# Optimization experiments

Hardware: AMD Instinct MI355X
Metric: run time of the kernel (lower is better)

Reference implementation:

```python
import jax, jax.numpy as jnp
import numpy as np

B, N_PIC, C, H, W, P = 32, 4, 3, 224, 224, 16
HP = H // P  # 14
NP = HP * HP  # 196 patches
D = C * P * P  # 768 = hidden_size


def setup_inputs() -> dict:
    key = jax.random.key(0)
    ks = jax.random.split(key, 12)
    s = 0.02
    def lin(k, din, dout):
        kw, kb = jax.random.split(k)
        return (jax.random.normal(kw, (din, dout), jnp.float32) * s,
                jax.random.normal(kb, (dout,), jnp.float32) * s)
    W1, b1 = lin(ks[0], D, D)
    Wq, bq = lin(ks[1], D, D)
    Wk, bk = lin(ks[2], D, D)
    Wv, bv = lin(ks[3], D, D)
    Wo1, bo1 = lin(ks[4], D, D)
    Wo2, bo2 = lin(ks[5], D, D)
    x = jax.random.normal(ks[6], (B, N_PIC, C, H, W), jnp.float32)
    return {"x": x, "W1": W1, "b1": b1, "Wq": Wq, "bq": bq, "Wk": Wk,
            "bk": bk, "Wv": Wv, "bv": bv, "Wo1": Wo1, "bo1": bo1,
            "Wo2": Wo2, "bo2": bo2}


def reference(x, W1, b1, Wq, bq, Wk, bk, Wv, bv, Wo1, bo1, Wo2, bo2):
    b = x.shape[0]
    # patchify: matches torch unfold(3,P,P).unfold(4,P,P) + permute + view
    # -> [b, N, num_patches, C*P*P] with (C, ph, pw) ordering in last dim
    p = x.reshape(b, N_PIC, C, HP, P, HP, P)
    p = p.transpose(0, 1, 3, 5, 2, 4, 6).reshape(b, N_PIC, NP, D)
    h = p @ W1 + b1  # [b, N, S, D]
    # attention: query always from picture 0; key/value per picture (batched)
    Q = h[:, 0] @ Wq + bq          # [b, S, D]
    K = h @ Wk + bk                # [b, N, S, D]
    V = h @ Wv + bv                # [b, N, S, D]
    scale = 1.0 / jnp.sqrt(jnp.float32(D))
    scores = jnp.einsum('bsd,bnmd->bnsm', Q, K) * scale  # [b, N, S, S]
    attn = jax.nn.softmax(scores, axis=-1)
    wv = jnp.einsum('bnsm,bnmd->bnsd', attn, V)           # [b, N, S, D]
    out = jax.nn.relu(wv @ Wo1 + bo1) @ Wo2 + bo2
    return out
```

## Files before the change

### kernel.cpp

```cpp
#include <hip/hip_runtime.h>

typedef __bf16 bf16;
typedef __bf16 bf16x8 __attribute__((ext_vector_type(8)));
typedef float  f32x4  __attribute__((ext_vector_type(4)));


__global__ __launch_bounds__(256) void patchify_k(const float* __restrict__ x,
                                                  bf16* __restrict__ p) {
  int t = blockIdx.x * 256 + threadIdx.x;
  if (t >= 128 * 3 * 14 * 16 * 14) return;
  int j  = t % 14; t /= 14;
  int ph = t % 16; t /= 16;
  int i  = t % 14; t /= 14;
  int c  = t % 3;  t /= 3;
  int bn = t;
  const float* src = x + (((long long)(bn * 3 + c) * 224 + (i * 16 + ph)) * 224 + j * 16);
  bf16* dst = p + ((long long)(bn * 196 + (i * 14 + j)) * 768 + c * 256 + ph * 16);
  bf16 tmp[16];
  for (int k = 0; k < 16; k += 4) {
    float4 f = *(const float4*)(src + k);
    tmp[k + 0] = (bf16)f.x; tmp[k + 1] = (bf16)f.y;
    tmp[k + 2] = (bf16)f.z; tmp[k + 3] = (bf16)f.w;
  }
  *(bf16x8*)(dst)     = *(bf16x8*)&tmp[0];
  *(bf16x8*)(dst + 8) = *(bf16x8*)&tmp[8];
}

__global__ __launch_bounds__(256) void wtrans_k(const float* __restrict__ w0,
                                                const float* __restrict__ w1,
                                                const float* __restrict__ w2,
                                                const float* __restrict__ w3,
                                                const float* __restrict__ w4,
                                                const float* __restrict__ w5,
                                                bf16* __restrict__ out) {
  __shared__ float tile[32][33];
  const float* W;
  switch (blockIdx.z) {
    case 0: W = w0; break; case 1: W = w1; break; case 2: W = w2; break;
    case 3: W = w3; break; case 4: W = w4; break; default: W = w5; break;
  }
  bf16* o = out + (long long)blockIdx.z * 768 * 768;
  int nb = blockIdx.x * 32, kb = blockIdx.y * 32;
  int c = threadIdx.x & 31, r = threadIdx.x >> 5;
  for (int rr = 0; rr < 32; rr += 8)
    tile[r + rr][c] = W[(long long)(kb + r + rr) * 768 + nb + c];
  __syncthreads();
  for (int rr = 0; rr < 32; rr += 8)
    o[(long long)(nb + r + rr) * 768 + kb + c] = (bf16)tile[c][r + rr];
}

__global__ __launch_bounds__(256) void vtrans_k(const bf16* __restrict__ kv,
                                                bf16* __restrict__ Vt) {
  __shared__ short tile[32][33];
  int z = blockIdx.z;
  const short* v = (const short*)(kv + (long long)z * 301056 + 768);
  short* vt = (short*)(Vt + (long long)z * 768 * 224);
  int db = blockIdx.x * 32;
  int mb = blockIdx.y * 32;
  int c = threadIdx.x & 31, r = threadIdx.x >> 5;
  for (int rr = 0; rr < 32; rr += 8) {
    int m = mb + r + rr;
    short val = 0;
    if (m < 196) val = v[(long long)m * 1536 + db + c];
    tile[r + rr][c] = val;
  }
  __syncthreads();
  for (int rr = 0; rr < 32; rr += 8) {
    int d = db + r + rr;
    vt[(long long)d * 224 + mb + c] = tile[c][r + rr];
  }
}

__global__ __launch_bounds__(64) void softmax_k(const float* __restrict__ S,
                                                bf16* __restrict__ attn) {
  const int row = blockIdx.x;
  const float* sr = S + (long long)row * 196;
  const int l = threadIdx.x;
  float v0 = sr[l];
  float v1 = sr[l + 64];
  float v2 = sr[l + 128];
  float v3 = (l + 192 < 196) ? sr[l + 192] : -1e30f;
  float mx = fmaxf(fmaxf(v0, v1), fmaxf(v2, v3));
  for (int o = 32; o > 0; o >>= 1) mx = fmaxf(mx, __shfl_xor(mx, o));
  float e0 = __expf(v0 - mx);
  float e1 = __expf(v1 - mx);
  float e2 = __expf(v2 - mx);
  float e3 = (l + 192 < 196) ? __expf(v3 - mx) : 0.f;
  float s = e0 + e1 + e2 + e3;
  for (int o = 32; o > 0; o >>= 1) s += __shfl_xor(s, o);
  float inv = 1.0f / s;
  bf16* ar = attn + (long long)row * 224;
  ar[l]       = (bf16)(e0 * inv);
  ar[l + 64]  = (bf16)(e1 * inv);
  ar[l + 128] = (bf16)(e2 * inv);
  int m3 = l + 192;
  if (m3 < 196) ar[m3] = (bf16)(e3 * inv);
  else if (m3 < 224) ar[m3] = (bf16)0.0f;
}

__device__ __forceinline__ void gld16(const bf16* g, bf16* l) {
  __builtin_amdgcn_global_load_lds(
      (const __attribute__((address_space(1))) unsigned int*)g,
      (__attribute__((address_space(3))) unsigned int*)l, 16, 0, 0);
}

__global__ __launch_bounds__(256) void gemm128(
    const bf16* __restrict__ A, const bf16* __restrict__ Bt,
    const float* __restrict__ bias, const float* __restrict__ bias2,
    void* __restrict__ Cout,
    int M, int N, int K, int lda, int ldb, int gr, long long gs,
    long long strideAz, int a_zdiv, long long strideBz, long long strideCz,
    float scale, int relu, int out_bf16) {
  __shared__ __align__(16) bf16 As[2][4096];
  __shared__ __align__(16) bf16 Bs[2][4096];

  const int tid = threadIdx.x;
  const int lane = tid & 63;
  const int w = tid >> 6;
  const int wm = w & 1, wn = w >> 1;
  const int z = blockIdx.z;
  const int n0 = blockIdx.x * 128, m0 = blockIdx.y * 128;

  const bf16* Az  = A  + (long long)(z / a_zdiv) * strideAz;
  const bf16* Btz = Bt + (long long)z * strideBz;

  const int r0 = tid >> 2, kc0 = (tid & 3) * 8;
  int ar0 = m0 + r0;       if (ar0 >= M) ar0 = M - 1;
  int ar1 = m0 + 64 + r0;  if (ar1 >= M) ar1 = M - 1;
  const bf16* aP0 = Az + (long long)(ar0 / gr) * gs + (long long)(ar0 % gr) * lda + kc0;
  const bf16* aP1 = Az + (long long)(ar1 / gr) * gs + (long long)(ar1 % gr) * lda + kc0;
  int br0 = n0 + r0;       if (br0 >= N) br0 = N - 1;
  int br1 = n0 + 64 + r0;  if (br1 >= N) br1 = N - 1;
  const bf16* bP0 = Btz + (long long)br0 * ldb + kc0;
  const bf16* bP1 = Btz + (long long)br1 * ldb + kc0;

  const int dstOff = w * 512;

  const int niter = K >> 5;
  f32x4 acc[4][4] = {};
  const int fr = lane & 15, fq = lane >> 4;

  gld16(aP0, As[0] + dstOff);
  gld16(aP1, As[0] + 2048 + dstOff);
  gld16(bP0, Bs[0] + dstOff);
  gld16(bP1, Bs[0] + 2048 + dstOff);

  for (int i = 0; i < niter; ++i) {
    __syncthreads();
    const int cur = i & 1;
    if (i + 1 < niter) {
      const int nb = cur ^ 1;
      const int off = (i + 1) << 5;
      gld16(aP0 + off, As[nb] + dstOff);
      gld16(aP1 + off, As[nb] + 2048 + dstOff);
      gld16(bP0 + off, Bs[nb] + dstOff);
      gld16(bP1 + off, Bs[nb] + 2048 + dstOff);
    }
    const bf16* Ac = As[cur];
    const bf16* Bc = Bs[cur];
    bf16x8 a[4], b[4];
#pragma unroll
    for (int mi = 0; mi < 4; mi++)
      a[mi] = *(const bf16x8*)&Ac[(wm * 64 + mi * 16 + fr) * 32 + fq * 8];
#pragma unroll
    for (int ni = 0; ni < 4; ni++)
      b[ni] = *(const bf16x8*)&Bc[(wn * 64 + ni * 16 + fr) * 32 + fq * 8];
#pragma unroll
    for (int mi = 0; mi < 4; mi++)
#pragma unroll
      for (int ni = 0; ni < 4; ni++)
        acc[mi][ni] = __builtin_amdgcn_mfma_f32_16x16x32_bf16(a[mi], b[ni], acc[mi][ni], 0, 0, 0);
  }

  const long long cz = (long long)z * strideCz;
#pragma unroll
  for (int ni = 0; ni < 4; ni++) {
    int col = n0 + wn * 64 + ni * 16 + fr;
    if (col >= N) continue;
    float bb = 0.f;
    if (bias) bb = (bias2 && col >= 768) ? bias2[col - 768] : bias[col];
#pragma unroll
    for (int mi = 0; mi < 4; mi++) {
      int rbase = m0 + wm * 64 + mi * 16 + fq * 4;
#pragma unroll
      for (int r = 0; r < 4; r++) {
        int row = rbase + r;
        if (row >= M) continue;
        float v = acc[mi][ni][r] * scale + bb;
        if (relu) v = fmaxf(v, 0.f);
        long long idx = cz + (long long)row * N + col;
        if (out_bf16) ((bf16*)Cout)[idx] = (bf16)v;
        else          ((float*)Cout)[idx] = v;
      }
    }
  }
}

extern "C" void kernel_launch(void* const* d_in, const int* in_sizes, int n_in,
                              void* d_out, int out_size, void* d_ws, size_t ws_size,
                              hipStream_t stream) {
  (void)in_sizes; (void)n_in; (void)out_size; (void)ws_size;
  const float* x   = (const float*)d_in[0];
  const float* W1  = (const float*)d_in[1];
  const float* b1  = (const float*)d_in[2];
  const float* Wq  = (const float*)d_in[3];
  const float* bq  = (const float*)d_in[4];
  const float* Wk  = (const float*)d_in[5];
  const float* bk  = (const float*)d_in[6];
  const float* Wv  = (const float*)d_in[7];
  const float* bv  = (const float*)d_in[8];
  const float* Wo1 = (const float*)d_in[9];
  const float* bo1 = (const float*)d_in[10];
  const float* Wo2 = (const float*)d_in[11];
  const float* bo2 = (const float*)d_in[12];

  char* ws = (char*)d_ws;
  bf16*  p    = (bf16*)(ws + 0);
  bf16*  vt   = (bf16*)(ws + 0);
  bf16*  h    = (bf16*)(ws + 44040192LL);
  bf16*  wv   = (bf16*)(ws + 44040192LL);
  bf16*  kv   = (bf16*)(ws + 82575360LL);
  bf16*  o1   = (bf16*)(ws + 82575360LL);
  float* sc   = (float*)(ws + 159645696LL);
  bf16*  q    = (bf16*)(ws + 179314688LL);
  bf16*  attn = (bf16*)(ws + 179314688LL);
  bf16*  wt   = (bf16*)(ws + 190554112LL);
  constexpr long long WSZ = 768LL * 768;

  const float qk_scale = 0.03608439182435161f;

  patchify_k<<<4704, 256, 0, stream>>>(x, p);
  wtrans_k<<<dim3(24, 24, 6), 256, 0, stream>>>(W1, Wk, Wv, Wq, Wo1, Wo2, wt);

  gemm128<<<dim3(6, 196, 1), 256, 0, stream>>>(p, wt + 0 * WSZ, b1, nullptr, h,
      25088, 768, 768, 768, 768, 25088, 0LL, 0LL, 1, 0LL, 0LL, 1.f, 0, 1);
  gemm128<<<dim3(12, 196, 1), 256, 0, stream>>>(h, wt + 1 * WSZ, bk, bv, kv,
      25088, 1536, 768, 768, 768, 25088, 0LL, 0LL, 1, 0LL, 0LL, 1.f, 0, 1);
  gemm128<<<dim3(6, 49, 1), 256, 0, stream>>>(h, wt + 3 * WSZ, bq, nullptr, q,
      6272, 768, 768, 768, 768, 196, 602112LL, 0LL, 1, 0LL, 0LL, 1.f, 0, 1);
  vtrans_k<<<dim3(24, 7, 128), 256, 0, stream>>>(kv, vt);
  gemm128<<<dim3(2, 2, 128), 256, 0, stream>>>(q, kv, nullptr, nullptr, sc,
      196, 196, 768, 768, 1536, 196, 0LL, 150528LL, 4, 301056LL, 38416LL,
      qk_scale, 0, 0);
  softmax_k<<<25088, 64, 0, stream>>>(sc, attn);
  gemm128<<<dim3(6, 2, 128), 256, 0, stream>>>(attn, vt, nullptr, nullptr, wv,
      196, 768, 224, 224, 224, 196, 0LL, 43904LL, 1, 172032LL, 150528LL,
      1.f, 0, 1);
  gemm128<<<dim3(6, 196, 1), 256, 0, stream>>>(wv, wt + 4 * WSZ, bo1, nullptr, o1,
      25088, 768, 768, 768, 768, 25088, 0LL, 0LL, 1, 0LL, 0LL, 1.f, 1, 1);
  gemm128<<<dim3(6, 196, 1), 256, 0, stream>>>(o1, wt + 5 * WSZ, bo2, nullptr,
      (float*)d_out,
      25088, 768, 768, 768, 768, 25088, 0LL, 0LL, 1, 0LL, 0LL, 1.f, 0, 0);
}
```

Baseline: 646.8 us.

## Triple-buffer GEMM LDS tiles with two-ahead async prefetch and vmcnt waits

Moves the gemm128 main loop from double to triple buffering in LDS. Each iteration now prefetches the tile two steps ahead and waits with a partial vmcnt wait (WAITVM(4)) plus a raw barrier, instead of a full __syncthreads drain. The aim is to keep more global-to-LDS loads in flight so memory latency overlaps the MFMA work. In exchange the kernel uses 1.5x the LDS, which can lower occupancy, and the tail iterations issue redundant loads of the last tile.

```diff
diff --git a/kernel.cpp b/kernel.cpp
--- a/kernel.cpp
+++ b/kernel.cpp
@@ -104,6 +104,8 @@
       (__attribute__((address_space(3))) unsigned int*)l, 16, 0, 0);
 }
 
+#define WAITVM(N) __builtin_amdgcn_s_waitcnt(0x0F70 | (N))
+
 __global__ __launch_bounds__(256) void gemm128(
     const bf16* __restrict__ A, const bf16* __restrict__ Bt,
     const float* __restrict__ bias, const float* __restrict__ bias2,
@@ -111,8 +113,8 @@
     int M, int N, int K, int lda, int ldb, int gr, long long gs,
     long long strideAz, int a_zdiv, long long strideBz, long long strideCz,
     float scale, int relu, int out_bf16) {
-  __shared__ __align__(16) bf16 As[2][4096];
-  __shared__ __align__(16) bf16 Bs[2][4096];
+  __shared__ __align__(16) bf16 As[3][4096];
+  __shared__ __align__(16) bf16 Bs[3][4096];
 
   const int tid = threadIdx.x;
   const int lane = tid & 63;
@@ -136,28 +138,29 @@
 
   const int dstOff = w * 512;
 
+#define ISSUE(t, s) do { const int _o = (t) << 5;          \
+    gld16(aP0 + _o, As[(s)] + dstOff);                     \
+    gld16(aP1 + _o, As[(s)] + 2048 + dstOff);              \
+    gld16(bP0 + _o, Bs[(s)] + dstOff);                     \
+    gld16(bP1 + _o, Bs[(s)] + 2048 + dstOff); } while (0)
+
   const int niter = K >> 5;
   f32x4 acc[4][4] = {};
   const int fr = lane & 15, fq = lane >> 4;
 
-  gld16(aP0, As[0] + dstOff);
-  gld16(aP1, As[0] + 2048 + dstOff);
-  gld16(bP0, Bs[0] + dstOff);
-  gld16(bP1, Bs[0] + 2048 + dstOff);
-
+  ISSUE(0, 0);
+  ISSUE(1, 1);
+
+  int slot = 0;
   for (int i = 0; i < niter; ++i) {
-    __syncthreads();
-    const int cur = i & 1;
-    if (i + 1 < niter) {
-      const int nb = cur ^ 1;
-      const int off = (i + 1) << 5;
-      gld16(aP0 + off, As[nb] + dstOff);
-      gld16(aP1 + off, As[nb] + 2048 + dstOff);
-      gld16(bP0 + off, Bs[nb] + dstOff);
-      gld16(bP1 + off, Bs[nb] + 2048 + dstOff);
-    }
-    const bf16* Ac = As[cur];
-    const bf16* Bc = Bs[cur];
+    WAITVM(4);
+    __builtin_amdgcn_s_barrier();
+    int pf = i + 2;  if (pf >= niter) pf = niter - 1;
+    int ps = slot + 2; if (ps >= 3) ps -= 3;
+    ISSUE(pf, ps);
+
+    const bf16* Ac = As[slot];
+    const bf16* Bc = Bs[slot];
     bf16x8 a[4], b[4];
 #pragma unroll
     for (int mi = 0; mi < 4; mi++)
@@ -170,7 +173,11 @@
 #pragma unroll
       for (int ni = 0; ni < 4; ni++)
         acc[mi][ni] = __builtin_amdgcn_mfma_f32_16x16x32_bf16(a[mi], b[ni], acc[mi][ni], 0, 0, 0);
-  }
+
+    slot = (slot == 2) ? 0 : slot + 1;
+  }
+  WAITVM(0);
+#undef ISSUE
 
   const long long cz = (long long)z * strideCz;
 #pragma unroll
```

Result: slower. 664.3 us (+2.7%).

## Rearrange GEMM LDS tile layout and stage epilogue through LDS for vector stores

Applied to the files above, without the earlier changes.

Changes the global-to-LDS load mapping so each wave writes 16-row by 32-k fragments in an MFMA-fragment-friendly order. Operand reads from LDS then become contiguous per lane group, which removes the row-stride bank conflicts of the old layout. The epilogue now writes bias/scale/relu results into LDS and stores them to global memory with 16-byte vector writes instead of scattered scalar stores. In exchange it adds barriers and a larger shared buffer, and the bf16 output path drops the column bounds check, so it relies on N being a multiple of 128.

```diff
diff --git a/kernel.cpp b/kernel.cpp
--- a/kernel.cpp
+++ b/kernel.cpp
@@ -111,8 +111,9 @@
     int M, int N, int K, int lda, int ldb, int gr, long long gs,
     long long strideAz, int a_zdiv, long long strideBz, long long strideCz,
     float scale, int relu, int out_bf16) {
-  __shared__ __align__(16) bf16 As[2][4096];
-  __shared__ __align__(16) bf16 Bs[2][4096];
+  __shared__ __align__(16) char smem[34816];
+  bf16* AsBuf = (bf16*)smem;
+  bf16* BsBuf = (bf16*)(smem + 16384);
 
   const int tid = threadIdx.x;
   const int lane = tid & 63;
@@ -124,74 +125,129 @@
   const bf16* Az  = A  + (long long)(z / a_zdiv) * strideAz;
   const bf16* Btz = Bt + (long long)z * strideBz;
 
-  const int r0 = tid >> 2, kc0 = (tid & 3) * 8;
-  int ar0 = m0 + r0;       if (ar0 >= M) ar0 = M - 1;
-  int ar1 = m0 + 64 + r0;  if (ar1 >= M) ar1 = M - 1;
-  const bf16* aP0 = Az + (long long)(ar0 / gr) * gs + (long long)(ar0 % gr) * lda + kc0;
-  const bf16* aP1 = Az + (long long)(ar1 / gr) * gs + (long long)(ar1 % gr) * lda + kc0;
-  int br0 = n0 + r0;       if (br0 >= N) br0 = N - 1;
-  int br1 = n0 + 64 + r0;  if (br1 >= N) br1 = N - 1;
-  const bf16* bP0 = Btz + (long long)br0 * ldb + kc0;
-  const bf16* bP1 = Btz + (long long)br1 * ldb + kc0;
+  const int rl  = 16 * w + (lane & 15);
+  const int kc8 = (lane >> 4) * 8;
+  int ar0 = m0 + rl;        if (ar0 >= M) ar0 = M - 1;
+  int ar1 = m0 + 64 + rl;   if (ar1 >= M) ar1 = M - 1;
+  const bf16* aP0 = Az + (long long)(ar0 / gr) * gs + (long long)(ar0 % gr) * lda + kc8;
+  const bf16* aP1 = Az + (long long)(ar1 / gr) * gs + (long long)(ar1 % gr) * lda + kc8;
+  int br0 = n0 + rl;        if (br0 >= N) br0 = N - 1;
+  int br1 = n0 + 64 + rl;   if (br1 >= N) br1 = N - 1;
+  const bf16* bP0 = Btz + (long long)br0 * ldb + kc8;
+  const bf16* bP1 = Btz + (long long)br1 * ldb + kc8;
 
   const int dstOff = w * 512;
+
+#define ISSUE(t, buf) do { const int _o = (t) << 5;                 \
+    gld16(aP0 + _o, AsBuf + (buf) * 4096 + dstOff);                 \
+    gld16(aP1 + _o, AsBuf + (buf) * 4096 + 2048 + dstOff);          \
+    gld16(bP0 + _o, BsBuf + (buf) * 4096 + dstOff);                 \
+    gld16(bP1 + _o, BsBuf + (buf) * 4096 + 2048 + dstOff); } while (0)
 
   const int niter = K >> 5;
   f32x4 acc[4][4] = {};
   const int fr = lane & 15, fq = lane >> 4;
 
-  gld16(aP0, As[0] + dstOff);
-  gld16(aP1, As[0] + 2048 + dstOff);
-  gld16(bP0, Bs[0] + dstOff);
-  gld16(bP1, Bs[0] + 2048 + dstOff);
+  ISSUE(0, 0);
 
   for (int i = 0; i < niter; ++i) {
     __syncthreads();
     const int cur = i & 1;
-    if (i + 1 < niter) {
-      const int nb = cur ^ 1;
-      const int off = (i + 1) << 5;
-      gld16(aP0 + off, As[nb] + dstOff);
-      gld16(aP1 + off, As[nb] + 2048 + dstOff);
-      gld16(bP0 + off, Bs[nb] + dstOff);
-      gld16(bP1 + off, Bs[nb] + 2048 + dstOff);
-    }
-    const bf16* Ac = As[cur];
-    const bf16* Bc = Bs[cur];
+    if (i + 1 < niter) ISSUE(i + 1, cur ^ 1);
+
+    const bf16* Ac = AsBuf + cur * 4096;
+    const bf16* Bc = BsBuf + cur * 4096;
     bf16x8 a[4], b[4];
 #pragma unroll
     for (int mi = 0; mi < 4; mi++)
-      a[mi] = *(const bf16x8*)&Ac[(wm * 64 + mi * 16 + fr) * 32 + fq * 8];
+      a[mi] = *(const bf16x8*)&Ac[(wm * 4 + mi) * 512 + fq * 128 + fr * 8];
 #pragma unroll
     for (int ni = 0; ni < 4; ni++)
-      b[ni] = *(const bf16x8*)&Bc[(wn * 64 + ni * 16 + fr) * 32 + fq * 8];
+      b[ni] = *(const bf16x8*)&Bc[(wn * 4 + ni) * 512 + fq * 128 + fr * 8];
 #pragma unroll
     for (int mi = 0; mi < 4; mi++)
 #pragma unroll
       for (int ni = 0; ni < 4; ni++)
         acc[mi][ni] = __builtin_amdgcn_mfma_f32_16x16x32_bf16(a[mi], b[ni], acc[mi][ni], 0, 0, 0);
   }
+#undef ISSUE
+
+  __syncthreads();
 
   const long long cz = (long long)z * strideCz;
-#pragma unroll
-  for (int ni = 0; ni < 4; ni++) {
-    int col = n0 + wn * 64 + ni * 16 + fr;
-    if (col >= N) continue;
-    float bb = 0.f;
-    if (bias) bb = (bias2 && col >= 768) ? bias2[col - 768] : bias[col];
-#pragma unroll
-    for (int mi = 0; mi < 4; mi++) {
-      int rbase = m0 + wm * 64 + mi * 16 + fq * 4;
-#pragma unroll
-      for (int r = 0; r < 4; r++) {
-        int row = rbase + r;
-        if (row >= M) continue;
-        float v = acc[mi][ni][r] * scale + bb;
-        if (relu) v = fmaxf(v, 0.f);
-        long long idx = cz + (long long)row * N + col;
-        if (out_bf16) ((bf16*)Cout)[idx] = (bf16)v;
-        else          ((float*)Cout)[idx] = v;
+  if (out_bf16) {
+    bf16* Cs = (bf16*)smem;
+#pragma unroll
+    for (int ni = 0; ni < 4; ni++) {
+      int col = wn * 64 + ni * 16 + fr;
+      int gcol = n0 + col;
+      float bb = 0.f;
+      if (bias) bb = (bias2 && gcol >= 768) ? bias2[gcol - 768] : bias[gcol];
+#pragma unroll
+      for (int mi = 0; mi < 4; mi++) {
+        int rbase = wm * 64 + mi * 16 + fq * 4;
+#pragma unroll
+        for (int r = 0; r < 4; r++) {
+          float v = acc[mi][ni][r] * scale + bb;
+          if (relu) v = fmaxf(v, 0.f);
+          Cs[(rbase + r) * 136 + col] = (bf16)v;
+        }
       }
+    }
+    __syncthreads();
+    bf16* Cp = (bf16*)Cout;
+    const int rr = tid >> 4, cc = (tid & 15) * 8;
+#pragma unroll
+    for (int pp = 0; pp < 8; pp++) {
+      int row = pp * 16 + rr;
+      int grow = m0 + row;
+      if (grow < M)
+        *(bf16x8*)(Cp + cz + (long long)grow * N + n0 + cc) =
+            *(const bf16x8*)&Cs[row * 136 + cc];
+    }
+  } else {
+    float* Cs = (float*)smem;
+    float* Cp = (float*)Cout;
+    for (int half = 0; half < 2; ++half) {
+      if (wm == half) {
+#pragma unroll
+        for (int ni = 0; ni < 4; ni++) {
+          int col = wn * 64 + ni * 16 + fr;
+          int gcol = n0 + col;
+          float bb = 0.f;
+          if (bias && gcol < N)
+            bb = (bias2 && gcol >= 768) ? bias2[gcol - 768] : bias[gcol];
+#pragma unroll
+          for (int mi = 0; mi < 4; mi++) {
+            int rbase = mi * 16 + fq * 4;
+#pragma unroll
+            for (int r = 0; r < 4; r++) {
+              float v = acc[mi][ni][r] * scale + bb;
+              if (relu) v = fmaxf(v, 0.f);
+              Cs[(rbase + r) * 132 + col] = v;
+            }
+          }
+        }
+      }
+      __syncthreads();
+      const int rr = tid >> 5, cc = (tid & 31) * 4;
+#pragma unroll
+      for (int pp = 0; pp < 8; pp++) {
+        int row = pp * 8 + rr;
+        int grow = m0 + half * 64 + row;
+        if (grow < M) {
+          int gcol = n0 + cc;
+          float* dst = Cp + cz + (long long)grow * N + gcol;
+          const float* srcl = &Cs[row * 132 + cc];
+          if (gcol + 4 <= N) {
+            *(float4*)dst = *(const float4*)srcl;
+          } else {
+            for (int e = 0; e < 4; e++)
+              if (gcol + e < N) dst[e] = srcl[e];
+          }
+        }
+      }
+      __syncthreads();
     }
   }
 }
```

Measured after the change: 602.7 us. 6.8% less time.
